# Kernel tuning notes

Measured on AMD Instinct MI355X. Metric: run time of the kernel, lower is better.

## Reference

```python
import jax, jax.numpy as jnp
import numpy as np

B, T, E = 2, 2048, 1024
H = 16            # num_heads (global in source repo)
D = E // H        # head_len
LN_EPS = 1e-5


def setup_inputs() -> dict:
    key = jax.random.key(0)
    ks = jax.random.split(key, 12)
    s = lambda fan_in: 1.0 / np.sqrt(fan_in)
    return {
        "x":     jax.random.normal(ks[0], (B, T, E), jnp.float32),
        "ln1_g": jnp.ones((E,), jnp.float32),
        "ln1_b": jnp.zeros((E,), jnp.float32),
        "Wq":    jax.random.normal(ks[1], (E, E), jnp.float32) * s(E),
        "Wk":    jax.random.normal(ks[2], (E, E), jnp.float32) * s(E),
        "Wv":    jax.random.normal(ks[3], (E, E), jnp.float32) * s(E),
        "Wo":    jax.random.normal(ks[4], (E, E), jnp.float32) * s(E),
        "bo":    jnp.zeros((E,), jnp.float32),
        "ln2_g": jnp.ones((E,), jnp.float32),
        "ln2_b": jnp.zeros((E,), jnp.float32),
        "W1":    jax.random.normal(ks[5], (E, 4 * E), jnp.float32) * s(E),
        "b1":    jnp.zeros((4 * E,), jnp.float32),
        "W2":    jax.random.normal(ks[6], (4 * E, E), jnp.float32) * s(4 * E),
        "b2":    jnp.zeros((E,), jnp.float32),
    }


def _layernorm(x, g, b):
    mu = jnp.mean(x, axis=-1, keepdims=True)
    var = jnp.mean(jnp.square(x - mu), axis=-1, keepdims=True)
    return (x - mu) * jax.lax.rsqrt(var + LN_EPS) * g + b


def _attention(x, Wq, Wk, Wv, Wo, bo):
    b, t, e = x.shape
    q = (x @ Wq).reshape(b, t, H, D)
    k = (x @ Wk).reshape(b, t, H, D)
    v = (x @ Wv).reshape(b, t, H, D)
    scores = jnp.einsum("bqhd,bkhd->bhqk", q, k) / np.sqrt(D).astype(np.float32)
    causal = jnp.tril(jnp.ones((t, t), bool))
    scores = jnp.where(causal, scores, -jnp.inf)
    attn = jax.nn.softmax(scores, axis=-1)
    out = jnp.einsum("bhqk,bkhd->bqhd", attn, v).reshape(b, t, e)
    return out @ Wo + bo


def reference(x, ln1_g, ln1_b, Wq, Wk, Wv, Wo, bo, ln2_g, ln2_b, W1, b1, W2, b2):
    # pre-norm attention + residual (dropout=0 / eval mode)
    x = x + _attention(_layernorm(x, ln1_g, ln1_b), Wq, Wk, Wv, Wo, bo)
    # pre-norm MLP + residual
    h = _layernorm(x, ln2_g, ln2_b)
    h = jax.nn.relu(h @ W1 + b1) @ W2 + b2
    return x + h
```

## Files before the change

kernel.cpp:

```cpp
#include <hip/hip_runtime.h>
#include <cmath>
#include <cstdint>
#include <cstddef>

typedef __bf16 bf16_t;
typedef __bf16 bf16x8 __attribute__((ext_vector_type(8)));
typedef float  f32x4  __attribute__((ext_vector_type(4)));

#define B_   2
#define T_   2048
#define E_   1024
#define H_   16
#define D_   64
#define FF_  4096
#define NROW (B_ * T_)
#define QS_  (3 * E_)
#define NTI  (T_ / 64)

__global__ __launch_bounds__(256) void ln_kernel(
    const float* __restrict__ x, const float* __restrict__ g,
    const float* __restrict__ bta, bf16_t* __restrict__ out)
{
    int row = blockIdx.x;
    int tid = threadIdx.x;
    const float4* xr = (const float4*)(x + (size_t)row * E_);
    float4 v = xr[tid];
    float s  = v.x + v.y + v.z + v.w;
    float ss = v.x * v.x + v.y * v.y + v.z * v.z + v.w * v.w;
#pragma unroll
    for (int off = 32; off; off >>= 1) {
        s  += __shfl_xor(s, off);
        ss += __shfl_xor(ss, off);
    }
    __shared__ float red[8];
    int wave = tid >> 6, lane = tid & 63;
    if (lane == 0) { red[wave] = s; red[4 + wave] = ss; }
    __syncthreads();
    s  = red[0] + red[1] + red[2] + red[3];
    ss = red[4] + red[5] + red[6] + red[7];
    float mu   = s * (1.0f / E_);
    float var  = ss * (1.0f / E_) - mu * mu;
    float rstd = rsqrtf(var + 1e-5f);
    float4 gv = ((const float4*)g)[tid];
    float4 bv = ((const float4*)bta)[tid];
    union { bf16_t h[4]; ushort4 u; } pk;
    pk.h[0] = (bf16_t)((v.x - mu) * rstd * gv.x + bv.x);
    pk.h[1] = (bf16_t)((v.y - mu) * rstd * gv.y + bv.y);
    pk.h[2] = (bf16_t)((v.z - mu) * rstd * gv.z + bv.z);
    pk.h[3] = (bf16_t)((v.w - mu) * rstd * gv.w + bv.w);
    ((ushort4*)(out + (size_t)row * E_))[tid] = pk.u;
}

__global__ __launch_bounds__(256) void ln_reduce2(
    const float* __restrict__ p, const float* __restrict__ bias,
    const float* __restrict__ resid, float* __restrict__ x1,
    const float* __restrict__ g, const float* __restrict__ bta,
    bf16_t* __restrict__ out)
{
    int row = blockIdx.x;
    int tid = threadIdx.x;
    size_t off = (size_t)row * E_;
    float4 v0 = ((const float4*)(p + off))[tid];
    float4 v1 = ((const float4*)(p + (size_t)NROW * E_ + off))[tid];
    float4 bb = ((const float4*)bias)[tid];
    float4 rr = ((const float4*)(resid + off))[tid];
    float4 v;
    v.x = v0.x + v1.x + bb.x + rr.x;
    v.y = v0.y + v1.y + bb.y + rr.y;
    v.z = v0.z + v1.z + bb.z + rr.z;
    v.w = v0.w + v1.w + bb.w + rr.w;
    ((float4*)(x1 + off))[tid] = v;
    float s  = v.x + v.y + v.z + v.w;
    float ss = v.x * v.x + v.y * v.y + v.z * v.z + v.w * v.w;
#pragma unroll
    for (int o = 32; o; o >>= 1) {
        s  += __shfl_xor(s, o);
        ss += __shfl_xor(ss, o);
    }
    __shared__ float red[8];
    int wave = tid >> 6, lane = tid & 63;
    if (lane == 0) { red[wave] = s; red[4 + wave] = ss; }
    __syncthreads();
    s  = red[0] + red[1] + red[2] + red[3];
    ss = red[4] + red[5] + red[6] + red[7];
    float mu   = s * (1.0f / E_);
    float var  = ss * (1.0f / E_) - mu * mu;
    float rstd = rsqrtf(var + 1e-5f);
    float4 gv = ((const float4*)g)[tid];
    float4 bv = ((const float4*)bta)[tid];
    union { bf16_t h[4]; ushort4 u; } pk;
    pk.h[0] = (bf16_t)((v.x - mu) * rstd * gv.x + bv.x);
    pk.h[1] = (bf16_t)((v.y - mu) * rstd * gv.y + bv.y);
    pk.h[2] = (bf16_t)((v.z - mu) * rstd * gv.z + bv.z);
    pk.h[3] = (bf16_t)((v.w - mu) * rstd * gv.w + bv.w);
    ((ushort4*)(out + off))[tid] = pk.u;
}

__global__ __launch_bounds__(256) void add_reduce2(
    const float* __restrict__ p, const float* __restrict__ bias,
    const float* __restrict__ resid, float* __restrict__ out)
{
    int row = blockIdx.x;
    int tid = threadIdx.x;
    size_t off = (size_t)row * E_;
    float4 v0 = ((const float4*)(p + off))[tid];
    float4 v1 = ((const float4*)(p + (size_t)NROW * E_ + off))[tid];
    float4 bb = ((const float4*)bias)[tid];
    float4 rr = ((const float4*)(resid + off))[tid];
    float4 v;
    v.x = v0.x + v1.x + bb.x + rr.x;
    v.y = v0.y + v1.y + bb.y + rr.y;
    v.z = v0.z + v1.z + bb.z + rr.z;
    v.w = v0.w + v1.w + bb.w + rr.w;
    ((float4*)(out + off))[tid] = v;
}

__global__ __launch_bounds__(256) void transpose_all(
    const float* __restrict__ Wq, const float* __restrict__ Wk,
    const float* __restrict__ Wv, const float* __restrict__ Wo,
    const float* __restrict__ W1, const float* __restrict__ W2,
    bf16_t* __restrict__ wqkv, bf16_t* __restrict__ wot,
    bf16_t* __restrict__ w1t, bf16_t* __restrict__ w2t)
{
    int l = blockIdx.x;
    const float* W; bf16_t* Wt; int K, N, bx, by;
    if (l < 4096) {
        int seg = l >> 10, r = l & 1023;
        K = E_; N = E_; bx = r & 31; by = r >> 5;
        if      (seg == 0) { W = Wq; Wt = wqkv; }
        else if (seg == 1) { W = Wk; Wt = wqkv + (size_t)E_ * E_; }
        else if (seg == 2) { W = Wv; Wt = wqkv + (size_t)2 * E_ * E_; }
        else               { W = Wo; Wt = wot; }
    } else if (l < 8192) {
        int r = l - 4096; K = E_; N = FF_; bx = r & 127; by = r >> 7;
        W = W1; Wt = w1t;
    } else {
        int r = l - 8192; K = FF_; N = E_; bx = r & 31; by = r >> 5;
        W = W2; Wt = w2t;
    }
    __shared__ float t[32][33];
    int n0 = bx * 32, k0 = by * 32;
    int tx = threadIdx.x & 31, ty = threadIdx.x >> 5;
#pragma unroll
    for (int i = 0; i < 4; ++i)
        t[ty + i * 8][tx] = W[(size_t)(k0 + ty + i * 8) * N + n0 + tx];
    __syncthreads();
#pragma unroll
    for (int i = 0; i < 4; ++i)
        Wt[(size_t)(n0 + ty + i * 8) * K + k0 + tx] = (bf16_t)t[tx][ty + i * 8];
}

#define BM 128
#define BN 128
#define BK 64

__device__ __forceinline__ void gload16(const bf16_t* g, bf16_t* l)
{
    __builtin_amdgcn_global_load_lds(
        (const __attribute__((address_space(1))) void*)g,
        (__attribute__((address_space(3))) void*)l, 16, 0, 0);
}

__global__ __launch_bounds__(256) void gemm_bt(
    const bf16_t* __restrict__ A, const bf16_t* __restrict__ Bt,
    const float* __restrict__ bias, const float* __restrict__ resid,
    void* __restrict__ Cout, bf16_t* __restrict__ vt_out,
    int M, int N, int K, int lda, int ldb,
    int has_bias, int do_relu, int has_resid, int out_bf16)
{
    __shared__ __attribute__((aligned(16))) bf16_t As[BM * BK];
    __shared__ __attribute__((aligned(16))) bf16_t Bs[BN * BK];
    int tid  = threadIdx.x;
    int lane = tid & 63, wave = tid >> 6;
    int m0 = blockIdx.x * BM, n0 = blockIdx.y * BN;
    int wm = (wave & 1) * 64, wn = (wave >> 1) * 64;
    int koff = blockIdx.z * K;
    f32x4 acc[4][4];
#pragma unroll
    for (int i = 0; i < 4; ++i)
#pragma unroll
        for (int j = 0; j < 4; ++j) acc[i][j] = (f32x4){0.f, 0.f, 0.f, 0.f};

    const int kq = (lane >> 4) * 8;
    const int ml = lane & 15;

    int srow = wave * 32 + (lane >> 3);
    int scol = (lane & 7) * 8;
    const bf16_t* Ag = A  + (size_t)(m0 + srow) * lda + koff + scol;
    const bf16_t* Bg = Bt + (size_t)(n0 + srow) * ldb + koff + scol;
    bf16_t* Asw = &As[wave * 32 * BK];
    bf16_t* Bsw = &Bs[wave * 32 * BK];
    int niter = K / BK;

#pragma unroll
    for (int j = 0; j < 4; ++j) {
        gload16(Ag + (size_t)j * 8 * lda, Asw + j * 8 * BK);
        gload16(Bg + (size_t)j * 8 * ldb, Bsw + j * 8 * BK);
    }

    for (int it = 0; it < niter; ++it) {
        __syncthreads();
#pragma unroll
        for (int ks = 0; ks < 2; ++ks) {
            bf16x8 af[4], bfr[4];
#pragma unroll
            for (int mi = 0; mi < 4; ++mi)
                af[mi] = *(const bf16x8*)&As[(wm + mi * 16 + ml) * BK + ks * 32 + kq];
#pragma unroll
            for (int ni = 0; ni < 4; ++ni)
                bfr[ni] = *(const bf16x8*)&Bs[(wn + ni * 16 + ml) * BK + ks * 32 + kq];
#pragma unroll
            for (int mi = 0; mi < 4; ++mi)
#pragma unroll
                for (int ni = 0; ni < 4; ++ni)
                    acc[mi][ni] = __builtin_amdgcn_mfma_f32_16x16x32_bf16(
                        af[mi], bfr[ni], acc[mi][ni], 0, 0, 0);
        }
        if (it + 1 < niter) {
            __syncthreads();
            int k0 = (it + 1) * BK;
#pragma unroll
            for (int j = 0; j < 4; ++j) {
                gload16(Ag + k0 + (size_t)j * 8 * lda, Asw + j * 8 * BK);
                gload16(Bg + k0 + (size_t)j * 8 * ldb, Bsw + j * 8 * BK);
            }
        }
    }

    int r4 = (lane >> 4) * 4;
    if (gridDim.z > 1) {
        float* P = (float*)Cout + (size_t)blockIdx.z * M * N;
#pragma unroll
        for (int mi = 0; mi < 4; ++mi)
#pragma unroll
            for (int ni = 0; ni < 4; ++ni) {
                int col = n0 + wn + ni * 16 + ml;
#pragma unroll
                for (int r = 0; r < 4; ++r) {
                    int row = m0 + wm + mi * 16 + r4 + r;
                    P[(size_t)row * N + col] = acc[mi][ni][r];
                }
            }
        return;
    }
    if (vt_out && n0 >= 2 * E_) {
#pragma unroll
        for (int mi = 0; mi < 4; ++mi)
#pragma unroll
            for (int ni = 0; ni < 4; ++ni) {
                int vcol = n0 + wn + ni * 16 + ml - 2 * E_;
                int h = vcol >> 6, d = vcol & 63;
                int row0 = m0 + wm + mi * 16 + r4;
                int b = row0 >> 11, t = row0 & (T_ - 1);
                union { bf16_t h4[4]; uint2 u; } pk;
#pragma unroll
                for (int r = 0; r < 4; ++r) pk.h4[r] = (bf16_t)acc[mi][ni][r];
                *(uint2*)&vt_out[((size_t)(b * H_ + h) * D_ + d) * T_ + t] = pk.u;
            }
        return;
    }
#pragma unroll
    for (int mi = 0; mi < 4; ++mi) {
#pragma unroll
        for (int ni = 0; ni < 4; ++ni) {
            int col = n0 + wn + ni * 16 + ml;
            float bval = has_bias ? bias[col] : 0.0f;
#pragma unroll
            for (int r = 0; r < 4; ++r) {
                int row = m0 + wm + mi * 16 + r4 + r;
                float v = acc[mi][ni][r] + bval;
                if (do_relu)   v = fmaxf(v, 0.0f);
                if (has_resid) v += resid[(size_t)row * N + col];
                if (out_bf16)
                    ((bf16_t*)Cout)[(size_t)row * N + col] = (bf16_t)v;
                else
                    ((float*)Cout)[(size_t)row * N + col] = v;
            }
        }
    }
}

#define PSTR 72

struct TileState {
    f32x4 acc[4];
    float m1, l1;
};

__device__ __forceinline__ void tile_update(
    const bf16x8 kf[2][4], const bf16x8 vf[2][4], const bf16x8 qf[2],
    TileState& st, bf16_t* PsW, int ml, int r4, int kq8,
    bool diag, int ch, int qrow)
{
    f32x4 s[4];
#pragma unroll
    for (int nt = 0; nt < 4; ++nt) {
        s[nt] = (f32x4){0.f, 0.f, 0.f, 0.f};
#pragma unroll
        for (int ks = 0; ks < 2; ++ks)
            s[nt] = __builtin_amdgcn_mfma_f32_16x16x32_bf16(kf[ks][nt], qf[ks], s[nt], 0, 0, 0);
    }
    if (diag) {
#pragma unroll
        for (int nt = 0; nt < 4; ++nt)
#pragma unroll
            for (int r = 0; r < 4; ++r)
                if (ch * 64 + nt * 16 + r4 + r > qrow) s[nt][r] = -INFINITY;
    }
    float mx = -INFINITY;
#pragma unroll
    for (int nt = 0; nt < 4; ++nt)
#pragma unroll
        for (int r = 0; r < 4; ++r) mx = fmaxf(mx, s[nt][r]);
    mx = fmaxf(mx, __shfl_xor(mx, 16));
    mx = fmaxf(mx, __shfl_xor(mx, 32));
    float mn = fmaxf(st.m1, mx);
    float al = __expf(st.m1 - mn);
    st.m1 = mn;
    float sum = 0.f;
#pragma unroll
    for (int nt = 0; nt < 4; ++nt)
#pragma unroll
        for (int r = 0; r < 4; ++r) {
            float p = __expf(s[nt][r] - mn);
            s[nt][r] = p;
            sum += p;
        }
    sum += __shfl_xor(sum, 16);
    sum += __shfl_xor(sum, 32);
    st.l1 = st.l1 * al + sum;
#pragma unroll
    for (int dt = 0; dt < 4; ++dt)
#pragma unroll
        for (int r = 0; r < 4; ++r) st.acc[dt][r] *= al;

#pragma unroll
    for (int nt = 0; nt < 4; ++nt) {
        union { bf16_t h[4]; uint2 u; } pk;
#pragma unroll
        for (int r = 0; r < 4; ++r) pk.h[r] = (bf16_t)s[nt][r];
        *(uint2*)&PsW[ml * PSTR + nt * 16 + r4] = pk.u;
    }
#pragma unroll
    for (int ks = 0; ks < 2; ++ks) {
        bf16x8 pf = *(const bf16x8*)&PsW[ml * PSTR + ks * 32 + kq8];
#pragma unroll
        for (int dt = 0; dt < 4; ++dt)
            st.acc[dt] = __builtin_amdgcn_mfma_f32_16x16x32_bf16(vf[ks][dt], pf, st.acc[dt], 0, 0, 0);
    }
}

__global__ __launch_bounds__(256) void attn_mfma(
    const bf16_t* __restrict__ Qp, const bf16_t* __restrict__ Kp,
    const bf16_t* __restrict__ Vt, bf16_t* __restrict__ O)
{
    __shared__ __attribute__((aligned(16))) bf16_t Ks[2][64 * PSTR];
    __shared__ __attribute__((aligned(16))) bf16_t Vts[2][64 * PSTR];
    __shared__ __attribute__((aligned(16))) bf16_t Ps[4][16 * PSTR];

    int tid = threadIdx.x, lane = tid & 63, wave = tid >> 6;
    int ml  = lane & 15;
    int kq8 = (lane >> 4) * 8;
    int r4  = (lane >> 4) * 4;
    int bh = blockIdx.y, b = bh >> 4, h = bh & 15;
    size_t qk_base = (size_t)b * T_ * QS_ + h * D_;
    size_t vt_base = (size_t)bh * D_ * T_;
    size_t o_base  = (size_t)b * T_ * E_ + h * D_;

    int lo = blockIdx.x, hi = NTI - 1 - blockIdx.x;
    int qlo = lo * 64 + wave * 16;
    int qhi = hi * 64 + wave * 16;

    bf16x8 qfl[2], qfh[2];
#pragma unroll
    for (int ks = 0; ks < 2; ++ks) {
        bf16x8 a = *(const bf16x8*)&Qp[qk_base + (size_t)(qlo + ml) * QS_ + ks * 32 + kq8];
        bf16x8 c = *(const bf16x8*)&Qp[qk_base + (size_t)(qhi + ml) * QS_ + ks * 32 + kq8];
#pragma unroll
        for (int j = 0; j < 8; ++j) {
            a[j] = (bf16_t)((float)a[j] * 0.125f);
            c[j] = (bf16_t)((float)c[j] * 0.125f);
        }
        qfl[ks] = a; qfh[ks] = c;
    }

    TileState stl, sth;
#pragma unroll
    for (int dt = 0; dt < 4; ++dt) {
        stl.acc[dt] = (f32x4){0.f, 0.f, 0.f, 0.f};
        sth.acc[dt] = (f32x4){0.f, 0.f, 0.f, 0.f};
    }
    stl.m1 = -INFINITY; stl.l1 = 0.f;
    sth.m1 = -INFINITY; sth.l1 = 0.f;

    int r0 = tid >> 3, c0 = (tid & 7) * 8;
    int nch = hi + 1;

    {
        const bf16_t* kb = &Kp[qk_base + (size_t)r0 * QS_ + c0];
        const bf16_t* vb = &Vt[vt_base + (size_t)r0 * T_ + c0];
        uint4 k0v = *(const uint4*)kb;
        uint4 k1v = *(const uint4*)(kb + (size_t)32 * QS_);
        uint4 v0v = *(const uint4*)vb;
        uint4 v1v = *(const uint4*)(vb + (size_t)32 * T_);
        *(uint4*)&Ks[0][r0 * PSTR + c0]         = k0v;
        *(uint4*)&Ks[0][(r0 + 32) * PSTR + c0]  = k1v;
        *(uint4*)&Vts[0][r0 * PSTR + c0]        = v0v;
        *(uint4*)&Vts[0][(r0 + 32) * PSTR + c0] = v1v;
    }

    for (int ch = 0; ch < nch; ++ch) {
        int cur = ch & 1, nxt = cur ^ 1;
        __syncthreads();

        uint4 nk0, nk1, nv0, nv1;
        bool pf = (ch + 1 < nch);
        if (pf) {
            const bf16_t* kb = &Kp[qk_base + (size_t)((ch + 1) * 64 + r0) * QS_ + c0];
            const bf16_t* vb = &Vt[vt_base + (size_t)r0 * T_ + (ch + 1) * 64 + c0];
            nk0 = *(const uint4*)kb;
            nk1 = *(const uint4*)(kb + (size_t)32 * QS_);
            nv0 = *(const uint4*)vb;
            nv1 = *(const uint4*)(vb + (size_t)32 * T_);
        }

        bf16x8 kf[2][4], vf[2][4];
#pragma unroll
        for (int ks = 0; ks < 2; ++ks)
#pragma unroll
            for (int nt = 0; nt < 4; ++nt) {
                kf[ks][nt] = *(const bf16x8*)&Ks[cur][(nt * 16 + ml) * PSTR + ks * 32 + kq8];
                vf[ks][nt] = *(const bf16x8*)&Vts[cur][(nt * 16 + ml) * PSTR + ks * 32 + kq8];
            }

        tile_update(kf, vf, qfh, sth, Ps[wave], ml, r4, kq8,
                    ch == hi, ch, qhi + ml);
        if (ch <= lo)
            tile_update(kf, vf, qfl, stl, Ps[wave], ml, r4, kq8,
                        ch == lo, ch, qlo + ml);

        if (pf) {
            *(uint4*)&Ks[nxt][r0 * PSTR + c0]         = nk0;
            *(uint4*)&Ks[nxt][(r0 + 32) * PSTR + c0]  = nk1;
            *(uint4*)&Vts[nxt][r0 * PSTR + c0]        = nv0;
            *(uint4*)&Vts[nxt][(r0 + 32) * PSTR + c0] = nv1;
        }
    }

#pragma unroll
    for (int t = 0; t < 2; ++t) {
        TileState& st = t ? stl : sth;
        int qw = t ? qlo : qhi;
        float inv = 1.0f / st.l1;
#pragma unroll
        for (int dt = 0; dt < 4; ++dt) {
            union { bf16_t h[4]; uint2 u; } pk;
#pragma unroll
            for (int r = 0; r < 4; ++r) pk.h[r] = (bf16_t)(st.acc[dt][r] * inv);
            *(uint2*)&Ps[wave][ml * PSTR + dt * 16 + r4] = pk.u;
        }
        int row = lane >> 2, seg = (lane & 3) * 16;
        bf16x8 o0 = *(const bf16x8*)&Ps[wave][row * PSTR + seg];
        bf16x8 o1 = *(const bf16x8*)&Ps[wave][row * PSTR + seg + 8];
        size_t gp = o_base + (size_t)(qw + row) * E_ + seg;
        *(bf16x8*)&O[gp]     = o0;
        *(bf16x8*)&O[gp + 8] = o1;
    }
}

extern "C" void kernel_launch(void* const* d_in, const int* in_sizes, int n_in,
                              void* d_out, int out_size, void* d_ws, size_t ws_size,
                              hipStream_t stream)
{
    const float* x    = (const float*)d_in[0];
    const float* ln1g = (const float*)d_in[1];
    const float* ln1b = (const float*)d_in[2];
    const float* Wq   = (const float*)d_in[3];
    const float* Wk   = (const float*)d_in[4];
    const float* Wv   = (const float*)d_in[5];
    const float* Wo   = (const float*)d_in[6];
    const float* bo   = (const float*)d_in[7];
    const float* ln2g = (const float*)d_in[8];
    const float* ln2b = (const float*)d_in[9];
    const float* W1   = (const float*)d_in[10];
    const float* b1   = (const float*)d_in[11];
    const float* W2   = (const float*)d_in[12];
    const float* b2   = (const float*)d_in[13];

    char* ws = (char*)d_ws;
    const size_t MB = 1024ull * 1024ull;
    bf16_t* wqkv = (bf16_t*)(ws + 0 * MB);
    bf16_t* wot  = (bf16_t*)(ws + 6 * MB);
    bf16_t* w1t  = (bf16_t*)(ws + 8 * MB);
    bf16_t* w2t  = (bf16_t*)(ws + 16 * MB);
    bf16_t* xn   = (bf16_t*)(ws + 24 * MB);
    bf16_t* QKV  = (bf16_t*)(ws + 32 * MB);
    bf16_t* att  = (bf16_t*)(ws + 56 * MB);
    float*  x1   = (float*)(ws + 64 * MB);
    bf16_t* hb   = (bf16_t*)(ws + 80 * MB);
    bf16_t* h1   = (bf16_t*)(ws + 88 * MB);
    bf16_t* Vtb  = (bf16_t*)(ws + 88 * MB);
    float*  part = (float*)(ws + 24 * MB);

    dim3 blk(256);

    transpose_all<<<dim3(12288), blk, 0, stream>>>(
        Wq, Wk, Wv, Wo, W1, W2, wqkv, wot, w1t, w2t);

    ln_kernel<<<dim3(NROW), blk, 0, stream>>>(x, ln1g, ln1b, xn);

    gemm_bt<<<dim3(NROW / BM, QS_ / BN), blk, 0, stream>>>(
        xn, wqkv, nullptr, nullptr, QKV, Vtb, NROW, QS_, E_, E_, E_, 0, 0, 0, 1);

    attn_mfma<<<dim3(NTI / 2, B_ * H_), blk, 0, stream>>>(
        QKV, QKV + E_, Vtb, att);

    gemm_bt<<<dim3(NROW / BM, E_ / BN, 2), blk, 0, stream>>>(
        att, wot, nullptr, nullptr, part, nullptr, NROW, E_, E_ / 2, E_, E_, 0, 0, 0, 0);
    ln_reduce2<<<dim3(NROW), blk, 0, stream>>>(
        part, bo, x, x1, ln2g, ln2b, hb);

    gemm_bt<<<dim3(NROW / BM, FF_ / BN), blk, 0, stream>>>(
        hb, w1t, b1, nullptr, h1, nullptr, NROW, FF_, E_, E_, E_, 1, 1, 0, 1);

    gemm_bt<<<dim3(NROW / BM, E_ / BN, 2), blk, 0, stream>>>(
        h1, w2t, nullptr, nullptr, part, nullptr, NROW, E_, FF_ / 2, FF_, FF_, 0, 0, 0, 0);
    add_reduce2<<<dim3(NROW), blk, 0, stream>>>(
        part, b2, x1, (float*)d_out);
}
```

Before: 357.5 us.

## Add 256x256 pipelined GEMM with direct-to-LDS loads for QKV and MLP

Adds a new 512-thread GEMM kernel with 256x256 tiles. It stages A and B through global_load_lds into XOR-swizzled, double-buffered LDS and interleaves the loads with MFMA phases under s_setprio. The QKV projection, W1 and W2 GEMMs now use it, and W2 moves to a 4-way split-K with a matching 4-way reduce kernel; the workspace layout is rearranged to fit the larger partial buffer. The aim is more data reuse per tile and better latency hiding for the large GEMMs, at the cost of 128KB of LDS per block, heavy register pressure and fewer blocks, which could hurt occupancy.

Result: faster. 333.2 us (-6.8%).

```diff
diff --git a/kernel.cpp b/kernel.cpp
--- a/kernel.cpp
+++ b/kernel.cpp
@@ -96,22 +96,25 @@
     ((ushort4*)(out + off))[tid] = pk.u;
 }
 
-__global__ __launch_bounds__(256) void add_reduce2(
+__global__ __launch_bounds__(256) void add_reduce4(
     const float* __restrict__ p, const float* __restrict__ bias,
     const float* __restrict__ resid, float* __restrict__ out)
 {
     int row = blockIdx.x;
     int tid = threadIdx.x;
     size_t off = (size_t)row * E_;
+    const size_t MN = (size_t)NROW * E_;
     float4 v0 = ((const float4*)(p + off))[tid];
-    float4 v1 = ((const float4*)(p + (size_t)NROW * E_ + off))[tid];
+    float4 v1 = ((const float4*)(p + MN + off))[tid];
+    float4 v2 = ((const float4*)(p + 2 * MN + off))[tid];
+    float4 v3 = ((const float4*)(p + 3 * MN + off))[tid];
     float4 bb = ((const float4*)bias)[tid];
     float4 rr = ((const float4*)(resid + off))[tid];
     float4 v;
-    v.x = v0.x + v1.x + bb.x + rr.x;
-    v.y = v0.y + v1.y + bb.y + rr.y;
-    v.z = v0.z + v1.z + bb.z + rr.z;
-    v.w = v0.w + v1.w + bb.w + rr.w;
+    v.x = (v0.x + v1.x) + (v2.x + v3.x) + bb.x + rr.x;
+    v.y = (v0.y + v1.y) + (v2.y + v3.y) + bb.y + rr.y;
+    v.z = (v0.z + v1.z) + (v2.z + v3.z) + bb.z + rr.z;
+    v.w = (v0.w + v1.w) + (v2.w + v3.w) + bb.w + rr.w;
     ((float4*)(out + off))[tid] = v;
 }
 
@@ -243,22 +246,6 @@
             }
         return;
     }
-    if (vt_out && n0 >= 2 * E_) {
-#pragma unroll
-        for (int mi = 0; mi < 4; ++mi)
-#pragma unroll
-            for (int ni = 0; ni < 4; ++ni) {
-                int vcol = n0 + wn + ni * 16 + ml - 2 * E_;
-                int h = vcol >> 6, d = vcol & 63;
-                int row0 = m0 + wm + mi * 16 + r4;
-                int b = row0 >> 11, t = row0 & (T_ - 1);
-                union { bf16_t h4[4]; uint2 u; } pk;
-#pragma unroll
-                for (int r = 0; r < 4; ++r) pk.h4[r] = (bf16_t)acc[mi][ni][r];
-                *(uint2*)&vt_out[((size_t)(b * H_ + h) * D_ + d) * T_ + t] = pk.u;
-            }
-        return;
-    }
 #pragma unroll
     for (int mi = 0; mi < 4; ++mi) {
 #pragma unroll
@@ -275,6 +262,211 @@
                     ((bf16_t*)Cout)[(size_t)row * N + col] = (bf16_t)v;
                 else
                     ((float*)Cout)[(size_t)row * N + col] = v;
+            }
+        }
+    }
+}
+
+
+__device__ __forceinline__ void g256_stage_half(
+    const bf16_t* gbase, int ldg, bf16_t* lhalf, int wave, int lane)
+{
+    int r = lane >> 3, c = lane & 7;
+    int sc = (c ^ r) * 8;
+#pragma unroll
+    for (int j = 0; j < 2; ++j) {
+        const bf16_t* src = gbase + (size_t)(wave * 8 + j * 64 + r) * ldg + sc;
+        bf16_t* dst = lhalf + (wave * 8 + j * 64) * 64;
+        __builtin_amdgcn_global_load_lds(
+            (const __attribute__((address_space(1))) void*)src,
+            (__attribute__((address_space(3))) void*)dst, 16, 0, 0);
+    }
+}
+
+__device__ __forceinline__ bf16x8 g256_frag(const bf16_t* half, int row, int kb)
+{
+    return *(const bf16x8*)((const char*)half + row * 128 + (kb ^ ((row & 7) << 4)));
+}
+
+template<int FP, bool DO_BFR>
+__device__ __forceinline__ void g256_reads(
+    const bf16_t* Ahx, const bf16_t* Bhx,
+    bf16x8 (&af)[2][2], bf16x8 (&bfr)[4][2],
+    int ml, int kq16, int brow0)
+{
+    if (DO_BFR) {
+#pragma unroll
+        for (int ni = 0; ni < 4; ++ni) {
+            bfr[ni][0] = g256_frag(Bhx, brow0 + ni * 16 + ml, kq16);
+            bfr[ni][1] = g256_frag(Bhx, brow0 + ni * 16 + ml, 64 + kq16);
+        }
+    }
+#pragma unroll
+    for (int i = 0; i < 2; ++i) {
+        af[i][0] = g256_frag(Ahx, (2 * FP + i) * 16 + ml, kq16);
+        af[i][1] = g256_frag(Ahx, (2 * FP + i) * 16 + ml, 64 + kq16);
+    }
+}
+
+template<int FP>
+__device__ __forceinline__ void g256_mfma(
+    const bf16x8 (&af)[2][2], const bf16x8 (&bfr)[4][2], f32x4 (&acc)[8][4])
+{
+    __builtin_amdgcn_s_setprio(1);
+#pragma unroll
+    for (int i = 0; i < 2; ++i)
+#pragma unroll
+        for (int ni = 0; ni < 4; ++ni)
+#pragma unroll
+            for (int ks = 0; ks < 2; ++ks)
+                acc[2 * FP + i][ni] = __builtin_amdgcn_mfma_f32_16x16x32_bf16(
+                    af[i][ks], bfr[ni][ks], acc[2 * FP + i][ni], 0, 0, 0);
+    __builtin_amdgcn_s_setprio(0);
+}
+
+#define AHALF(t, h) (ldsr + ((((t) & 1) * 4 + (h)) * (128 * 64)))
+#define BHALF(t, h) (ldsr + ((((t) & 1) * 4 + 2 + (h)) * (128 * 64)))
+#define STG_A(t, h) g256_stage_half(Ab + (size_t)((h) * 128) * lda + (t) * 64, lda, AHALF(t, h), wave, lane)
+#define STG_B(t, h) g256_stage_half(Bb + (size_t)((h) * 128) * ldb + (t) * 64, ldb, BHALF(t, h), wave, lane)
+#define SBAR() __builtin_amdgcn_s_barrier()
+
+__global__ __launch_bounds__(512, 2) void gemm256(
+    const bf16_t* __restrict__ A, const bf16_t* __restrict__ Bt,
+    const float* __restrict__ bias,
+    void* __restrict__ Cout, bf16_t* __restrict__ vt_out,
+    int M, int N, int K, int lda, int ldb,
+    int has_bias, int do_relu, int split)
+{
+    extern __shared__ __attribute__((aligned(16))) bf16_t ldsr[];
+    int tid = threadIdx.x, lane = tid & 63, wave = tid >> 6;
+    int m0 = blockIdx.x * 256, n0 = blockIdx.y * 256;
+    int koff = blockIdx.z * K;
+    int ml = lane & 15, kq16 = (lane >> 4) * 16, r4 = (lane >> 4) * 4;
+    int wr = (wave >> 2) * 128, wc = (wave & 3) * 64;
+    int brow0 = (wave & 1) * 64;
+
+    const bf16_t* Ab = A  + (size_t)m0 * lda + koff;
+    const bf16_t* Bb = Bt + (size_t)n0 * ldb + koff;
+
+    const bf16_t* A0 = AHALF(0, wave >> 2);
+    const bf16_t* A1 = AHALF(1, wave >> 2);
+    const bf16_t* B0 = BHALF(0, (wave & 3) >> 1);
+    const bf16_t* B1 = BHALF(1, (wave & 3) >> 1);
+
+    f32x4 acc[8][4];
+#pragma unroll
+    for (int i = 0; i < 8; ++i)
+#pragma unroll
+        for (int j = 0; j < 4; ++j) acc[i][j] = (f32x4){0.f, 0.f, 0.f, 0.f};
+    bf16x8 bfr[4][2];
+
+    STG_B(0, 0); STG_B(0, 1);
+    STG_A(0, 0); STG_A(0, 1);
+    STG_B(1, 0); STG_B(1, 1);
+    asm volatile("s_waitcnt vmcnt(4)" ::: "memory");
+    SBAR();
+
+    int NIT2 = K / 128;
+    for (int it = 0; it < NIT2; ++it) {
+        bool last = (it == NIT2 - 1);
+        int t1 = 2 * it + 1, t2 = 2 * it + 2, t3 = 2 * it + 3;
+        bf16x8 af[2][2];
+
+        g256_reads<0, true>(A0, B0, af, bfr, ml, kq16, brow0);
+        STG_A(t1, 0);
+        SBAR();
+        g256_mfma<0>(af, bfr, acc);
+        SBAR();
+
+        g256_reads<1, false>(A0, B0, af, bfr, ml, kq16, brow0);
+        STG_A(t1, 1);
+        SBAR();
+        g256_mfma<1>(af, bfr, acc);
+        SBAR();
+
+        g256_reads<2, false>(A0, B0, af, bfr, ml, kq16, brow0);
+        if (!last) STG_B(t2, 0);
+        SBAR();
+        g256_mfma<2>(af, bfr, acc);
+        SBAR();
+
+        g256_reads<3, false>(A0, B0, af, bfr, ml, kq16, brow0);
+        if (!last) STG_B(t2, 1);
+        SBAR();
+        g256_mfma<3>(af, bfr, acc);
+        if (last) asm volatile("s_waitcnt vmcnt(0)" ::: "memory");
+        else      asm volatile("s_waitcnt vmcnt(4)" ::: "memory");
+        SBAR();
+
+        g256_reads<0, true>(A1, B1, af, bfr, ml, kq16, brow0);
+        if (!last) STG_A(t2, 0);
+        SBAR();
+        g256_mfma<0>(af, bfr, acc);
+        SBAR();
+
+        g256_reads<1, false>(A1, B1, af, bfr, ml, kq16, brow0);
+        if (!last) STG_A(t2, 1);
+        SBAR();
+        g256_mfma<1>(af, bfr, acc);
+        SBAR();
+
+        g256_reads<2, false>(A1, B1, af, bfr, ml, kq16, brow0);
+        if (!last) STG_B(t3, 0);
+        SBAR();
+        g256_mfma<2>(af, bfr, acc);
+        SBAR();
+
+        g256_reads<3, false>(A1, B1, af, bfr, ml, kq16, brow0);
+        if (!last) STG_B(t3, 1);
+        SBAR();
+        g256_mfma<3>(af, bfr, acc);
+        if (!last) asm volatile("s_waitcnt vmcnt(4)" ::: "memory");
+        SBAR();
+    }
+
+    if (split > 1) {
+        float* P = (float*)Cout + (size_t)blockIdx.z * M * N;
+#pragma unroll
+        for (int mi = 0; mi < 8; ++mi)
+#pragma unroll
+            for (int ni = 0; ni < 4; ++ni) {
+                int col = n0 + wc + ni * 16 + ml;
+#pragma unroll
+                for (int r = 0; r < 4; ++r) {
+                    int row = m0 + wr + mi * 16 + r4 + r;
+                    P[(size_t)row * N + col] = acc[mi][ni][r];
+                }
+            }
+        return;
+    }
+    if (vt_out && n0 >= 2 * E_) {
+#pragma unroll
+        for (int mi = 0; mi < 8; ++mi)
+#pragma unroll
+            for (int ni = 0; ni < 4; ++ni) {
+                int vcol = n0 + wc + ni * 16 + ml - 2 * E_;
+                int h = vcol >> 6, d = vcol & 63;
+                int row0 = m0 + wr + mi * 16 + r4;
+                int b = row0 >> 11, t = row0 & (T_ - 1);
+                union { bf16_t h4[4]; uint2 u; } pk;
+#pragma unroll
+                for (int r = 0; r < 4; ++r) pk.h4[r] = (bf16_t)acc[mi][ni][r];
+                *(uint2*)&vt_out[((size_t)(b * H_ + h) * D_ + d) * T_ + t] = pk.u;
+            }
+        return;
+    }
+#pragma unroll
+    for (int mi = 0; mi < 8; ++mi) {
+#pragma unroll
+        for (int ni = 0; ni < 4; ++ni) {
+            int col = n0 + wc + ni * 16 + ml;
+            float bval = has_bias ? bias[col] : 0.0f;
+#pragma unroll
+            for (int r = 0; r < 4; ++r) {
+                int row = m0 + wr + mi * 16 + r4 + r;
+                float v = acc[mi][ni][r] + bval;
+                if (do_relu) v = fmaxf(v, 0.0f);
+                ((bf16_t*)Cout)[(size_t)row * N + col] = (bf16_t)v;
             }
         }
     }
@@ -489,42 +681,44 @@
 
     char* ws = (char*)d_ws;
     const size_t MB = 1024ull * 1024ull;
-    bf16_t* wqkv = (bf16_t*)(ws + 0 * MB);
-    bf16_t* wot  = (bf16_t*)(ws + 6 * MB);
-    bf16_t* w1t  = (bf16_t*)(ws + 8 * MB);
-    bf16_t* w2t  = (bf16_t*)(ws + 16 * MB);
-    bf16_t* xn   = (bf16_t*)(ws + 24 * MB);
-    bf16_t* QKV  = (bf16_t*)(ws + 32 * MB);
-    bf16_t* att  = (bf16_t*)(ws + 56 * MB);
-    float*  x1   = (float*)(ws + 64 * MB);
-    bf16_t* hb   = (bf16_t*)(ws + 80 * MB);
-    bf16_t* h1   = (bf16_t*)(ws + 88 * MB);
-    bf16_t* Vtb  = (bf16_t*)(ws + 88 * MB);
-    float*  part = (float*)(ws + 24 * MB);
-
-    dim3 blk(256);
+    bf16_t* w2t     = (bf16_t*)(ws + 0 * MB);
+    float*  x1      = (float*)(ws + 8 * MB);
+    float*  part_wo = (float*)(ws + 24 * MB);
+    bf16_t* h1      = (bf16_t*)(ws + 24 * MB);
+    bf16_t* w1t     = (bf16_t*)(ws + 56 * MB);
+    bf16_t* xn      = (bf16_t*)(ws + 64 * MB);
+    bf16_t* hb      = (bf16_t*)(ws + 64 * MB);
+    bf16_t* wqkv    = (bf16_t*)(ws + 72 * MB);
+    bf16_t* wot     = (bf16_t*)(ws + 78 * MB);
+    bf16_t* QKV     = (bf16_t*)(ws + 80 * MB);
+    bf16_t* Vtb     = (bf16_t*)(ws + 104 * MB);
+    bf16_t* att     = (bf16_t*)(ws + 112 * MB);
+    float*  part4   = (float*)(ws + 56 * MB);
+
+    dim3 blk(256), blk5(512);
+    const size_t LDS256 = 8 * 128 * 64 * sizeof(bf16_t);
 
     transpose_all<<<dim3(12288), blk, 0, stream>>>(
         Wq, Wk, Wv, Wo, W1, W2, wqkv, wot, w1t, w2t);
 
     ln_kernel<<<dim3(NROW), blk, 0, stream>>>(x, ln1g, ln1b, xn);
 
-    gemm_bt<<<dim3(NROW / BM, QS_ / BN), blk, 0, stream>>>(
-        xn, wqkv, nullptr, nullptr, QKV, Vtb, NROW, QS_, E_, E_, E_, 0, 0, 0, 1);
+    gemm256<<<dim3(NROW / 256, QS_ / 256, 1), blk5, LDS256, stream>>>(
+        xn, wqkv, nullptr, QKV, Vtb, NROW, QS_, E_, E_, E_, 0, 0, 1);
 
     attn_mfma<<<dim3(NTI / 2, B_ * H_), blk, 0, stream>>>(
         QKV, QKV + E_, Vtb, att);
 
     gemm_bt<<<dim3(NROW / BM, E_ / BN, 2), blk, 0, stream>>>(
-        att, wot, nullptr, nullptr, part, nullptr, NROW, E_, E_ / 2, E_, E_, 0, 0, 0, 0);
+        att, wot, nullptr, nullptr, part_wo, nullptr, NROW, E_, E_ / 2, E_, E_, 0, 0, 0, 0);
     ln_reduce2<<<dim3(NROW), blk, 0, stream>>>(
-        part, bo, x, x1, ln2g, ln2b, hb);
-
-    gemm_bt<<<dim3(NROW / BM, FF_ / BN), blk, 0, stream>>>(
-        hb, w1t, b1, nullptr, h1, nullptr, NROW, FF_, E_, E_, E_, 1, 1, 0, 1);
-
-    gemm_bt<<<dim3(NROW / BM, E_ / BN, 2), blk, 0, stream>>>(
-        h1, w2t, nullptr, nullptr, part, nullptr, NROW, E_, FF_ / 2, FF_, FF_, 0, 0, 0, 0);
-    add_reduce2<<<dim3(NROW), blk, 0, stream>>>(
-        part, b2, x1, (float*)d_out);
-}
+        part_wo, bo, x, x1, ln2g, ln2b, hb);
+
+    gemm256<<<dim3(NROW / 256, FF_ / 256, 1), blk5, LDS256, stream>>>(
+        hb, w1t, b1, h1, nullptr, NROW, FF_, E_, E_, E_, 1, 1, 1);
+
+    gemm256<<<dim3(NROW / 256, E_ / 256, 4), blk5, LDS256, stream>>>(
+        h1, w2t, nullptr, part4, nullptr, NROW, E_, FF_ / 4, FF_, FF_, 0, 0, 4);
+    add_reduce4<<<dim3(NROW), blk, 0, stream>>>(
+        part4, b2, x1, (float*)d_out);
+}
```
